# Optimization experiments

Measured on AMD Instinct MI355X. Metric: run time of the kernel, lower is better.

## Reference

```python
import jax, jax.numpy as jnp
import numpy as np

KH, KW, PAD = 3, 3, 1
K = KH * KW


def _offset_conv(x, w, b):
    # standard 3x3 conv, stride 1, padding 1, NCHW
    out = jax.lax.conv_general_dilated(
        x, w, window_strides=(1, 1), padding=((PAD, PAD), (PAD, PAD)),
        dimension_numbers=("NCHW", "OIHW", "NCHW"))
    return out + b[None, :, None, None]


def _deform_conv(x, offsets, weight, groups):
    # torchvision.ops.deform_conv2d semantics: offset channels are
    # (dy, dx) pairs per kernel tap; zero padding outside the image;
    # bilinear interpolation with per-corner validity masks.
    B, C, H, W = x.shape
    off = offsets.reshape(B, K, 2, H, W)
    dy, dx = off[:, :, 0], off[:, :, 1]                      # [B,K,H,W]

    ky, kx = jnp.meshgrid(jnp.arange(KH), jnp.arange(KW), indexing="ij")
    ky = ky.reshape(K); kx = kx.reshape(K)
    base_y = (jnp.arange(H)[None, :, None] + (ky - PAD)[:, None, None])  # [K,H,1]
    base_x = (jnp.arange(W)[None, None, :] + (kx - PAD)[:, None, None])  # [K,1,W]
    py = base_y[None].astype(x.dtype) + dy                   # [B,K,H,W]
    px = base_x[None].astype(x.dtype) + dx

    # torchvision returns 0 when the sample point is fully outside
    valid = (py > -1) & (py < H) & (px > -1) & (px < W)
    y0 = jnp.floor(py); x0 = jnp.floor(px)
    ly = py - y0; lx = px - x0                               # fractional parts
    y0i = y0.astype(jnp.int32); x0i = x0.astype(jnp.int32)

    def gather(yi, xi):
        ok = (yi >= 0) & (yi < H) & (xi >= 0) & (xi < W) & valid
        yic = jnp.clip(yi, 0, H - 1)
        xic = jnp.clip(xi, 0, W - 1)
        def per_b(img, yb, xb, okb):
            # img [C,H,W]; yb,xb,okb [K,H,W] -> [C,K,H,W]
            return img[:, yb, xb] * okb[None].astype(img.dtype)
        return jax.vmap(per_b)(x, yic, xic, ok)

    v00 = gather(y0i, x0i)
    v01 = gather(y0i, x0i + 1)
    v10 = gather(y0i + 1, x0i)
    v11 = gather(y0i + 1, x0i + 1)
    w00 = ((1 - ly) * (1 - lx))[:, None]
    w01 = ((1 - ly) * lx)[:, None]
    w10 = (ly * (1 - lx))[:, None]
    w11 = (ly * lx)[:, None]
    sampled = v00 * w00 + v01 * w01 + v10 * w10 + v11 * w11  # [B,C,K,H,W]

    Cg = C // groups
    sampled = sampled.reshape(B, groups, Cg, K, H, W)
    wg = weight.reshape(groups, Cg, Cg, K)                   # [G, Cout_g, Cin_g, K]
    out = jnp.einsum("bgckhw,gock->bgohw", sampled, wg)
    return out.reshape(B, C, H, W)


def setup_inputs() -> dict:
    key = jax.random.key(0)
    k1, k2, k3, k4 = jax.random.split(key, 4)
    B, C, H, W, groups = 4, 256, 96, 96, 4
    x = jax.random.normal(k1, (B, C, H, W), dtype=jnp.float32)
    # small offset-conv weights keep learned offsets in a realistic range
    offset_w = jax.random.normal(k2, (2 * K, C, KH, KW), dtype=jnp.float32) * 0.02
    offset_b = jax.random.normal(k3, (2 * K,), dtype=jnp.float32) * 0.1
    fan_in = (C // groups) * KH * KW
    weight = jax.random.normal(k4, (C, C // groups, KH, KW), dtype=jnp.float32) / np.sqrt(fan_in)
    return {"x": x, "offset_w": offset_w, "offset_b": offset_b,
            "weight": weight, "groups": groups}


def reference(x, offset_w, offset_b, weight, groups):
    offsets = _offset_conv(x, offset_w, offset_b)
    return _deform_conv(x, offsets, weight, groups)
```

## Files before the change

### kernel.cpp

```cpp
#include <hip/hip_runtime.h>
#include <hip/hip_bf16.h>
#include <math.h>

#define B_   4
#define C_   256
#define H_   96
#define W_   96
#define HW_  (H_ * W_)
#define G_   4
#define CG_  64
#define K_   9
#define PW_  98
#define PROW_ (PW_ * C_)

typedef __bf16  bf16x8 __attribute__((ext_vector_type(8)));
typedef float   f32x4  __attribute__((ext_vector_type(4)));

__global__ __launch_bounds__(256) void prep_kernel(
    const float* __restrict__ ow, const float* __restrict__ wt,
    __hip_bfloat16* __restrict__ aOW, __hip_bfloat16* __restrict__ aW)
{
    int idx = blockIdx.x * 256 + threadIdx.x;
    if (idx < 73728) {
        int j    = idx & 7;
        int r    = idx >> 3;
        int lane = r & 63;  r >>= 6;
        int mt   = r & 1;   r >>= 1;
        int ks   = r & 7;   r >>= 3;
        int tap  = r;
        int m = mt * 16 + (lane & 15);
        int c = ks * 32 + (lane >> 4) * 8 + j;
        float v = (m < 18) ? ow[(m * 256 + c) * 9 + tap] : 0.f;
        aOW[idx] = __float2bfloat16(v);
    }
    if (idx < 147456) {
        int j    = idx & 7;
        int r    = idx >> 3;
        int lane = r & 63;  r >>= 6;
        int ct   = r & 1;   r >>= 1;
        int half = r & 1;   r >>= 1;
        int ks   = r & 1;   r >>= 1;
        int tap  = r % 9;
        int g    = r / 9;
        int c  = ks * 32 + (lane >> 4) * 8 + j;
        int co = half * 32 + ct * 16 + (lane & 15);
        float v = wt[(((g * CG_ + co) * CG_ + c) * 9) + tap];
        aW[idx] = __float2bfloat16(v);
    }
}

__global__ __launch_bounds__(256) void transpose_kernel(
    const float* __restrict__ x, __hip_bfloat16* __restrict__ xtp)
{
    int blk = blockIdx.x;
    int ch  = blk & 1;
    int bh  = blk >> 1;
    int b = bh / H_, h = bh - b * H_;
    int t = threadIdx.x;
    __shared__ __align__(16) __hip_bfloat16 tile[96 * 136];
    const float* xb = x + (size_t)b * C_ * HW_ + (size_t)(ch * 128) * HW_ + h * W_;
    for (int r = 0; r < 48; ++r) {
        int e = r * 256 + t;
        int c = e / 96, w = e - c * 96;
        tile[w * 136 + c] = __float2bfloat16(xb[c * HW_ + w]);
    }
    __syncthreads();
    __hip_bfloat16* ob = xtp + ((size_t)(b * PW_ + h + 1) * PW_ + 1) * C_ + ch * 128;
#pragma unroll
    for (int i = 0; i < 6; ++i) {
        int sIdx = i * 256 + t;
        int px = sIdx >> 4, seg = sIdx & 15;
        *(bf16x8*)(ob + px * 256 + seg * 8) =
            *(const bf16x8*)(&tile[px * 136 + seg * 8]);
    }
    bf16x8 z = {};
    if (t < 32) {
        int side = t >> 4, i = t & 15;
        *(bf16x8*)(xtp + ((size_t)(b * PW_ + h + 1) * PW_ + side * 97) * C_
                   + ch * 128 + i * 8) = z;
    }
    if (h == 0 || h == 95) {
        int row = (h == 0) ? 0 : 97;
        __hip_bfloat16* rb = xtp + (size_t)(b * PW_ + row) * PROW_;
        for (int i = 0; i < 7; ++i) {
            int idx = i * 256 + t;
            if (idx < 1568) *(bf16x8*)(rb + (ch * 1568 + idx) * 8) = z;
        }
    }
}

__global__ __launch_bounds__(384) void offset_conv_kernel(
    const __hip_bfloat16* __restrict__ xtp, const __hip_bfloat16* __restrict__ aOW,
    const float* __restrict__ bias, __hip_bfloat16* __restrict__ off2)
{
    int blk = blockIdx.x;
    int xcd = blk & 7;
    int s   = blk >> 3;
    int unit = xcd * 96 + s;
    int bh   = unit >> 1;
    int whalf = unit & 1;
    int b   = bh / H_, h = bh % H_;
    int t = threadIdx.x, lane = t & 63;
    int ww = __builtin_amdgcn_readfirstlane(t >> 6);
    int nt = ww % 3;
    int kh = ww / 3;
    int w0 = whalf * 48 + nt * 16;
    int ml = lane & 15, kq = lane >> 4;

    __shared__ __align__(16) __hip_bfloat16 aS[2][8192];
    __shared__ __align__(16) f32x4 red[3 * 64 * 2];

    auto stage = [&](int tap, int p) {
        const bf16x8* src = (const bf16x8*)(aOW + tap * 8192);
        bf16x8* dst = (bf16x8*)aS[p];
        for (int i = t; i < 1024; i += 384) dst[i] = src[i];
    };

    f32x4 acc0 = {}, acc1 = {};
    const __hip_bfloat16* xb = xtp + (size_t)b * (PW_ * PROW_);

    stage(0, 0);
    __syncthreads();
    for (int tap = 0; tap < 9; ++tap) {
        if (tap < 8) stage(tap + 1, (tap + 1) & 1);
        int ky = tap / 3, kx = tap - ky * 3;
        const __hip_bfloat16* brow =
            xb + ((h + ky) * PW_ + (w0 + ml + kx)) * C_ + kh * 128 + kq * 8;
        const __hip_bfloat16* arow = aS[tap & 1] + kh * 4096 + lane * 8;
#pragma unroll
        for (int ks = 0; ks < 4; ++ks) {
            bf16x8 bf = *(const bf16x8*)(brow + ks * 32);
            bf16x8 a0 = *(const bf16x8*)(arow + ks * 1024);
            bf16x8 a1 = *(const bf16x8*)(arow + ks * 1024 + 512);
            acc0 = __builtin_amdgcn_mfma_f32_16x16x32_bf16(a0, bf, acc0, 0, 0, 0);
            acc1 = __builtin_amdgcn_mfma_f32_16x16x32_bf16(a1, bf, acc1, 0, 0, 0);
        }
        __syncthreads();
    }

    if (kh == 1) {
        red[(nt * 64 + lane) * 2 + 0] = acc0;
        red[(nt * 64 + lane) * 2 + 1] = acc1;
    }
    __syncthreads();
    if (kh == 0) {
        acc0 += red[(nt * 64 + lane) * 2 + 0];
        acc1 += red[(nt * 64 + lane) * 2 + 1];
        int w = w0 + ml;
#pragma unroll
        for (int r = 0; r < 4; ++r) {
            int j0 = kq * 4 + r;
            off2[((size_t)(b * 9 + (j0 >> 1)) * HW_ + h * W_ + w) * 2 + (j0 & 1)] =
                __float2bfloat16(acc0[r] + bias[j0]);
            int j1 = 16 + kq * 4 + r;
            if (j1 < 18)
                off2[((size_t)(b * 9 + (j1 >> 1)) * HW_ + h * W_ + w) * 2 + (j1 & 1)] =
                    __float2bfloat16(acc1[r] + bias[j1]);
        }
    }
}

__global__ __launch_bounds__(384, 6) void deform_kernel(
    const __hip_bfloat16* __restrict__ xtp, const __hip_bfloat16* __restrict__ off2,
    const __hip_bfloat16* __restrict__ aW, float* __restrict__ out)
{
    int blk = blockIdx.x;
    int xcd = blk & 7;
    int s   = blk >> 3;
    int bg  = xcd * 2 + (s / H_);
    int h   = s % H_;
    int g   = bg & 3;
    int b   = bg >> 2;
    int t    = threadIdx.x;
    int lane = t & 63;
    int wave = __builtin_amdgcn_readfirstlane(t >> 6);
    int half   = wave & 1;
    int wthird = wave >> 1;

    __shared__ __align__(16) __hip_bfloat16 sS[2][96 * 72];

    const __hip_bfloat16* xb =
        xtp + ((size_t)b * (PW_ * PW_) + PW_ + 1) * C_ + g * CG_;
    const __hip_bfloat162* offp =
        (const __hip_bfloat162*)off2 + (size_t)(b * 9) * HW_ + h * W_;
    const __hip_bfloat16* aWg = aW + (g * 9) * 4096;

    int tw8 = t >> 3;
    int j8  = (t & 7) * 8;

    f32x4 acc[2][2] = {};

    __hip_bfloat162 pr[2];
    bf16x8 c00[2], c01[2], c10[2], c11[2];
    float bw00[2], bw01[2], bw10[2], bw11[2];

    auto ld_off = [&](int k) {
#pragma unroll
        for (int it = 0; it < 2; ++it)
            pr[it] = offp[k * HW_ + it * 48 + tw8];
    };

    auto gather = [&](int k) {
        int ky = k / 3, kx = k - ky * 3;
#pragma unroll
        for (int it = 0; it < 2; ++it) {
            int w  = it * 48 + tw8;
            float py = (float)(h + ky - 1) + __bfloat162float(pr[it].x);
            float px = (float)(w + kx - 1) + __bfloat162float(pr[it].y);
            bool valid = (py > -1.f) && (py < (float)H_) &&
                         (px > -1.f) && (px < (float)W_);
            float y0f = floorf(py), x0f = floorf(px);
            float ly = py - y0f, lx = px - x0f;
            int y0 = (int)y0f, x0 = (int)x0f;
            int base = valid ? (y0 * PW_ + x0) * C_ : -(PW_ + 1) * C_;
            float wy1 = valid ? ly : 0.f;
            float wy0 = valid ? (1.f - ly) : 0.f;
            float mx0 = 1.f - lx;
            bw00[it] = wy0 * mx0; bw01[it] = wy0 * lx;
            bw10[it] = wy1 * mx0; bw11[it] = wy1 * lx;
            const __hip_bfloat16* p0 = xb + base + j8;
            c00[it] = *(const bf16x8*)(p0);
            c01[it] = *(const bf16x8*)(p0 + C_);
            c10[it] = *(const bf16x8*)(p0 + PROW_);
            c11[it] = *(const bf16x8*)(p0 + PROW_ + C_);
        }
    };

    auto finish = [&](int p) {
#pragma unroll
        for (int it = 0; it < 2; ++it) {
            int w = it * 48 + tw8;
            bf16x8 r;
#pragma unroll
            for (int e = 0; e < 8; ++e) {
                float v = bw00[it] * (float)c00[it][e] + bw01[it] * (float)c01[it][e]
                        + bw10[it] * (float)c10[it][e] + bw11[it] * (float)c11[it][e];
                r[e] = (__bf16)v;
            }
            *(bf16x8*)(&sS[p][w * 72 + j8]) = r;
        }
    };

    auto mmtap = [&](int k, int p) {
        const __hip_bfloat16* at = aWg + k * 4096 + half * 1024 + lane * 8;
#pragma unroll
        for (int ks = 0; ks < 2; ++ks) {
            bf16x8 a0 = *(const bf16x8*)(at + ks * 2048);
            bf16x8 a1 = *(const bf16x8*)(at + ks * 2048 + 512);
#pragma unroll
            for (int wt = 0; wt < 2; ++wt) {
                int wrow = wthird * 32 + wt * 16 + (lane & 15);
                bf16x8 bfrag = *(const bf16x8*)(
                    &sS[p][wrow * 72 + ks * 32 + (lane >> 4) * 8]);
                acc[0][wt] = __builtin_amdgcn_mfma_f32_16x16x32_bf16(
                                 a0, bfrag, acc[0][wt], 0, 0, 0);
                acc[1][wt] = __builtin_amdgcn_mfma_f32_16x16x32_bf16(
                                 a1, bfrag, acc[1][wt], 0, 0, 0);
            }
        }
    };

    ld_off(0);
    gather(0);
    ld_off(1);
    finish(0);
    __syncthreads();

#pragma unroll
    for (int k = 0; k < K_; ++k) {
        if (k < K_ - 1) {
            gather(k + 1);
            if (k < K_ - 2) ld_off(k + 2);
        }
        mmtap(k, k & 1);
        if (k < K_ - 1) {
            finish((k + 1) & 1);
            __syncthreads();
        }
    }

    float* ob = out + ((b * C_ + g * CG_ + half * 32) * HW_) + h * W_ + wthird * 32;
    int rbase = (lane >> 4) * 4;
    int ncol  = lane & 15;
#pragma unroll
    for (int ct = 0; ct < 2; ++ct)
#pragma unroll
        for (int wt = 0; wt < 2; ++wt)
#pragma unroll
            for (int r = 0; r < 4; ++r)
                __builtin_nontemporal_store(
                    acc[ct][wt][r],
                    ob + (ct * 16 + rbase + r) * HW_ + wt * 16 + ncol);
}

extern "C" void kernel_launch(void* const* d_in, const int* in_sizes, int n_in,
                              void* d_out, int out_size, void* d_ws, size_t ws_size,
                              hipStream_t stream) {
    const float* x    = (const float*)d_in[0];
    const float* ow   = (const float*)d_in[1];
    const float* obi  = (const float*)d_in[2];
    const float* wt   = (const float*)d_in[3];

    __hip_bfloat16* xtp  = (__hip_bfloat16*)d_ws;
    __hip_bfloat16* off2 = xtp + (size_t)B_ * PW_ * PW_ * C_;
    __hip_bfloat16* aW   = off2 + (size_t)B_ * 9 * HW_ * 2;
    __hip_bfloat16* aOW  = aW + 147456;

    prep_kernel<<<576, 256, 0, stream>>>(ow, wt, aOW, aW);
    transpose_kernel<<<B_ * H_ * 2, 256, 0, stream>>>(x, xtp);
    offset_conv_kernel<<<B_ * H_ * 2, 384, 0, stream>>>(xtp, aOW, obi, off2);
    deform_kernel<<<B_ * G_ * H_, 384, 0, stream>>>(xtp, off2, aW, (float*)d_out);
}
```

Baseline: 187.9 us.

## Make deform conv wave-independent, gathering bilinear samples straight into MFMA fragments

The deform kernel previously had a block of six waves share a 96-pixel row. It staged interpolated samples through double-buffered LDS with a barrier per tap. Now each wave owns a 16-pixel by 64-channel tile and builds its MFMA B fragments directly in registers from the gathered corners, which removes shared memory and all __syncthreads. The cost is that each wave reloads all weight A fragments per tap, with no sharing across waves, and the software pipelining between gather and matmul is gone. The block size and grid are changed to match.

```diff
diff --git a/kernel.cpp b/kernel.cpp
--- a/kernel.cpp
+++ b/kernel.cpp
@@ -160,137 +160,89 @@
     }
 }
 
-__global__ __launch_bounds__(384, 6) void deform_kernel(
+__global__ __launch_bounds__(256, 4) void deform_kernel(
     const __hip_bfloat16* __restrict__ xtp, const __hip_bfloat16* __restrict__ off2,
     const __hip_bfloat16* __restrict__ aW, float* __restrict__ out)
 {
     int blk = blockIdx.x;
     int xcd = blk & 7;
-    int s   = blk >> 3;
-    int bg  = xcd * 2 + (s / H_);
-    int h   = s % H_;
+    int unit = xcd * 288 + (blk >> 3);
+    int wv  = __builtin_amdgcn_readfirstlane(threadIdx.x >> 6);
+    int task = unit * 4 + wv;
+    int wt  = task % 6;
+    int r0  = task / 6;
+    int h   = r0 % H_;
+    int bg  = r0 / H_;
     int g   = bg & 3;
     int b   = bg >> 2;
-    int t    = threadIdx.x;
-    int lane = t & 63;
-    int wave = __builtin_amdgcn_readfirstlane(t >> 6);
-    int half   = wave & 1;
-    int wthird = wave >> 1;
-
-    __shared__ __align__(16) __hip_bfloat16 sS[2][96 * 72];
+    int lane = threadIdx.x & 63;
+    int wq = lane >> 4;
+    int wn = lane & 15;
+    int w  = wt * 16 + wn;
 
     const __hip_bfloat16* xb =
-        xtp + ((size_t)b * (PW_ * PW_) + PW_ + 1) * C_ + g * CG_;
+        xtp + ((size_t)b * (PW_ * PW_) + PW_ + 1) * C_ + g * CG_ + wq * 8;
     const __hip_bfloat162* offp =
-        (const __hip_bfloat162*)off2 + (size_t)(b * 9) * HW_ + h * W_;
-    const __hip_bfloat16* aWg = aW + (g * 9) * 4096;
-
-    int tw8 = t >> 3;
-    int j8  = (t & 7) * 8;
-
-    f32x4 acc[2][2] = {};
-
-    __hip_bfloat162 pr[2];
-    bf16x8 c00[2], c01[2], c10[2], c11[2];
-    float bw00[2], bw01[2], bw10[2], bw11[2];
-
-    auto ld_off = [&](int k) {
-#pragma unroll
-        for (int it = 0; it < 2; ++it)
-            pr[it] = offp[k * HW_ + it * 48 + tw8];
-    };
-
-    auto gather = [&](int k) {
+        (const __hip_bfloat162*)off2 + (size_t)(b * 9) * HW_ + h * W_ + w;
+    const __hip_bfloat16* aWg = aW + (size_t)(g * 9) * 4096 + lane * 8;
+
+    f32x4 acc[4] = {};
+
+    __hip_bfloat162 pr[9];
+#pragma unroll
+    for (int k = 0; k < 9; ++k) pr[k] = offp[k * HW_];
+
+#pragma unroll
+    for (int k = 0; k < 9; ++k) {
         int ky = k / 3, kx = k - ky * 3;
-#pragma unroll
-        for (int it = 0; it < 2; ++it) {
-            int w  = it * 48 + tw8;
-            float py = (float)(h + ky - 1) + __bfloat162float(pr[it].x);
-            float px = (float)(w + kx - 1) + __bfloat162float(pr[it].y);
-            bool valid = (py > -1.f) && (py < (float)H_) &&
-                         (px > -1.f) && (px < (float)W_);
-            float y0f = floorf(py), x0f = floorf(px);
-            float ly = py - y0f, lx = px - x0f;
-            int y0 = (int)y0f, x0 = (int)x0f;
-            int base = valid ? (y0 * PW_ + x0) * C_ : -(PW_ + 1) * C_;
-            float wy1 = valid ? ly : 0.f;
-            float wy0 = valid ? (1.f - ly) : 0.f;
-            float mx0 = 1.f - lx;
-            bw00[it] = wy0 * mx0; bw01[it] = wy0 * lx;
-            bw10[it] = wy1 * mx0; bw11[it] = wy1 * lx;
-            const __hip_bfloat16* p0 = xb + base + j8;
-            c00[it] = *(const bf16x8*)(p0);
-            c01[it] = *(const bf16x8*)(p0 + C_);
-            c10[it] = *(const bf16x8*)(p0 + PROW_);
-            c11[it] = *(const bf16x8*)(p0 + PROW_ + C_);
-        }
-    };
-
-    auto finish = [&](int p) {
-#pragma unroll
-        for (int it = 0; it < 2; ++it) {
-            int w = it * 48 + tw8;
-            bf16x8 r;
+        float py = (float)(h + ky - 1) + __bfloat162float(pr[k].x);
+        float px = (float)(w + kx - 1) + __bfloat162float(pr[k].y);
+        bool valid = (py > -1.f) && (py < (float)H_) &&
+                     (px > -1.f) && (px < (float)W_);
+        float y0f = floorf(py), x0f = floorf(px);
+        float ly = py - y0f, lx = px - x0f;
+        int y0 = (int)y0f, x0 = (int)x0f;
+        int base = valid ? (y0 * PW_ + x0) * C_ : -(PW_ + 1) * C_;
+        float wy1 = valid ? ly : 0.f;
+        float wy0 = valid ? (1.f - ly) : 0.f;
+        float mx0 = 1.f - lx;
+        float bw00 = wy0 * mx0, bw01 = wy0 * lx;
+        float bw10 = wy1 * mx0, bw11 = wy1 * lx;
+        const __hip_bfloat16* p0 = xb + base;
+
+        bf16x8 bfrag[2];
+#pragma unroll
+        for (int ks = 0; ks < 2; ++ks) {
+            const __hip_bfloat16* pk = p0 + ks * 32;
+            bf16x8 c00 = *(const bf16x8*)(pk);
+            bf16x8 c01 = *(const bf16x8*)(pk + C_);
+            bf16x8 c10 = *(const bf16x8*)(pk + PROW_);
+            bf16x8 c11 = *(const bf16x8*)(pk + PROW_ + C_);
 #pragma unroll
             for (int e = 0; e < 8; ++e) {
-                float v = bw00[it] * (float)c00[it][e] + bw01[it] * (float)c01[it][e]
-                        + bw10[it] * (float)c10[it][e] + bw11[it] * (float)c11[it][e];
-                r[e] = (__bf16)v;
+                float v = bw00 * (float)c00[e] + bw01 * (float)c01[e]
+                        + bw10 * (float)c10[e] + bw11 * (float)c11[e];
+                bfrag[ks][e] = (__bf16)v;
             }
-            *(bf16x8*)(&sS[p][w * 72 + j8]) = r;
-        }
-    };
-
-    auto mmtap = [&](int k, int p) {
-        const __hip_bfloat16* at = aWg + k * 4096 + half * 1024 + lane * 8;
-#pragma unroll
-        for (int ks = 0; ks < 2; ++ks) {
-            bf16x8 a0 = *(const bf16x8*)(at + ks * 2048);
-            bf16x8 a1 = *(const bf16x8*)(at + ks * 2048 + 512);
-#pragma unroll
-            for (int wt = 0; wt < 2; ++wt) {
-                int wrow = wthird * 32 + wt * 16 + (lane & 15);
-                bf16x8 bfrag = *(const bf16x8*)(
-                    &sS[p][wrow * 72 + ks * 32 + (lane >> 4) * 8]);
-                acc[0][wt] = __builtin_amdgcn_mfma_f32_16x16x32_bf16(
-                                 a0, bfrag, acc[0][wt], 0, 0, 0);
-                acc[1][wt] = __builtin_amdgcn_mfma_f32_16x16x32_bf16(
-                                 a1, bfrag, acc[1][wt], 0, 0, 0);
+        }
+
+        const __hip_bfloat16* at = aWg + k * 4096;
+#pragma unroll
+        for (int ks = 0; ks < 2; ++ks)
+#pragma unroll
+            for (int hc = 0; hc < 4; ++hc) {
+                bf16x8 af = *(const bf16x8*)(at + ks * 2048 + hc * 512);
+                acc[hc] = __builtin_amdgcn_mfma_f32_16x16x32_bf16(
+                              af, bfrag[ks], acc[hc], 0, 0, 0);
             }
-        }
-    };
-
-    ld_off(0);
-    gather(0);
-    ld_off(1);
-    finish(0);
-    __syncthreads();
-
-#pragma unroll
-    for (int k = 0; k < K_; ++k) {
-        if (k < K_ - 1) {
-            gather(k + 1);
-            if (k < K_ - 2) ld_off(k + 2);
-        }
-        mmtap(k, k & 1);
-        if (k < K_ - 1) {
-            finish((k + 1) & 1);
-            __syncthreads();
-        }
-    }
-
-    float* ob = out + ((b * C_ + g * CG_ + half * 32) * HW_) + h * W_ + wthird * 32;
-    int rbase = (lane >> 4) * 4;
-    int ncol  = lane & 15;
-#pragma unroll
-    for (int ct = 0; ct < 2; ++ct)
-#pragma unroll
-        for (int wt = 0; wt < 2; ++wt)
-#pragma unroll
-            for (int r = 0; r < 4; ++r)
-                __builtin_nontemporal_store(
-                    acc[ct][wt][r],
-                    ob + (ct * 16 + rbase + r) * HW_ + wt * 16 + ncol);
+    }
+
+    float* ob = out + ((size_t)(b * C_ + g * CG_ + wq * 4)) * HW_ + h * W_ + w;
+#pragma unroll
+    for (int hc = 0; hc < 4; ++hc)
+#pragma unroll
+        for (int rr = 0; rr < 4; ++rr)
+            __builtin_nontemporal_store(acc[hc][rr], ob + (hc * 16 + rr) * HW_);
 }
 
 extern "C" void kernel_launch(void* const* d_in, const int* in_sizes, int n_in,
@@ -309,5 +261,5 @@
     prep_kernel<<<576, 256, 0, stream>>>(ow, wt, aOW, aW);
     transpose_kernel<<<B_ * H_ * 2, 256, 0, stream>>>(x, xtp);
     offset_conv_kernel<<<B_ * H_ * 2, 384, 0, stream>>>(xtp, aOW, obi, off2);
-    deform_kernel<<<B_ * G_ * H_, 384, 0, stream>>>(xtp, off2, aW, (float*)d_out);
-}
+    deform_kernel<<<B_ * G_ * H_ * 6 / 4, 256, 0, stream>>>(xtp, off2, aW, (float*)d_out);
+}
```

Measured after the change: 215.5 us. +14.7%, slower.
